# Performance work log

Measured on AMD Instinct MI355X. Metric: run time of the kernel, lower is better.

The kernel has to match this reference:

```python
import jax, jax.numpy as jnp
import numpy as np

B, U, D = 128, 200, 512

def setup_inputs() -> dict:
    key = jax.random.key(0)
    k1, k2, k3 = jax.random.split(key, 3)
    input_real = jax.random.normal(k1, (B, D, D), dtype=jnp.float32)
    input_imag = jax.random.normal(k2, (B, D, D), dtype=jnp.float32)
    # keras 'uniform' initializer: U(-0.05, 0.05); unit_norm constraint normalizes over axes (1,2)
    kernel = jax.random.uniform(k3, (U, D, 2), dtype=jnp.float32, minval=-0.05, maxval=0.05)
    kernel = kernel / jnp.linalg.norm(kernel.reshape(U, -1), axis=1)[:, None, None]
    return {"input_real": input_real, "input_imag": input_imag, "kernel": kernel}

def reference(input_real, input_imag, kernel):
    # kernel: [U, D, 2] -> real/imag measurement vectors
    kr = kernel[:, :, 0]  # [U, D]
    ki = kernel[:, :, 1]  # [U, D]
    # Original: M_real = kr kr^T - ki ki^T ; M_imag = ki kr^T + kr ki^T (outer products per unit)
    # out[b,n] = trace(R_b @ M_real_n) - trace(I_b @ M_imag_n)
    # trace(A @ (u v^T)) = sum_ij A[i,j] u[j] v[i] -> quadratic form, avoids [B,U,D,D] tiles.
    t_real = (jnp.einsum('bij,nj,ni->bn', input_real, kr, kr)
              - jnp.einsum('bij,nj,ni->bn', input_real, ki, ki))
    t_imag = (jnp.einsum('bij,nj,ni->bn', input_imag, ki, kr)
              + jnp.einsum('bij,nj,ni->bn', input_imag, kr, ki))
    return t_real - t_imag  # [B, U]
```

## Files before the change

kernel.cpp:

```cpp
#include <hip/hip_runtime.h>
#include <hip/hip_bf16.h>
#include <string.h>

#define BB 128
#define UU 200
#define DD 512
#define NP 256

typedef __attribute__((ext_vector_type(8))) short short8;
typedef __attribute__((ext_vector_type(4))) float f32x4;
typedef __attribute__((ext_vector_type(16))) float f32x16;

__device__ __forceinline__ unsigned pack_bf16_2(float a, float b) {
    __hip_bfloat162 h = __float22bfloat162_rn(make_float2(a, b));
    unsigned u; memcpy(&u, &h, 4); return u;
}

__device__ __forceinline__ unsigned short f2bf(float x) {
    union { float f; unsigned u; } v; v.f = x;
    unsigned r = v.u + 0x7FFFu + ((v.u >> 16) & 1u);
    return (unsigned short)(r >> 16);
}

__device__ __forceinline__ void glds16(const float* g, float* l) {
    __builtin_amdgcn_global_load_lds(
        (const __attribute__((address_space(1))) unsigned*)g,
        (__attribute__((address_space(3))) unsigned*)l, 16, 0, 0);
}

__global__ void kb2_build_kernel(const float* __restrict__ Kt,
                                 unsigned short* __restrict__ Kbr,
                                 unsigned short* __restrict__ Kbi,
                                 float* __restrict__ out) {
    int idx = blockIdx.x * 256 + threadIdx.x;
    int n = idx >> 9, j = idx & 511;
    unsigned short r = 0, im = 0;
    if (n < UU) {
        float2 s = ((const float2*)Kt)[(size_t)n * DD + j];
        r = f2bf(s.x); im = f2bf(s.y);
    }
    Kbr[idx] = r;
    Kbi[idx] = im;
    if (idx < BB * UU) out[idx] = 0.0f;
}

__global__ void zero_out_kernel(float* __restrict__ out) {
    int i = blockIdx.x * 256 + threadIdx.x;
    if (i < BB * UU) out[i] = 0.0f;
}

__global__ __launch_bounds__(512, 5) void qf_gemm_kernel(
    const float* __restrict__ Ar, const float* __restrict__ Ai,
    const float* __restrict__ Kt,
    const unsigned short* __restrict__ Kbr, const unsigned short* __restrict__ Kbi,
    float* __restrict__ out)
{
    __shared__ float sAf[2][2][32 * 64];

    const int tid  = threadIdx.x;
    const int bx   = blockIdx.x;
    const int b    = bx >> 4;
    const int i0   = (bx & 15) * 32;

    const int w    = tid >> 6;
    const int lane = tid & 63;
    const int l31  = lane & 31;
    const int h    = lane >> 5;
    const int key  = l31 & 15;

    const int srow = w * 4 + (lane >> 4);
    const int scol = (lane & 15) ^ (srow & 15);
    const float* gR = Ar + ((size_t)b * DD + i0 + srow) * DD + scol * 4;
    const float* gI = Ai + ((size_t)b * DD + i0 + srow) * DD + scol * 4;
    const int ldsbase = w * 4 * 64;

    const unsigned short* kbrp = Kbr + (size_t)(w * 32 + l31) * 512 + h * 8;
    const unsigned short* kbip = Kbi + (size_t)(w * 32 + l31) * 512 + h * 8;

    const int rb = l31 * 64;
    int off0[4];
#pragma unroll
    for (int ks = 0; ks < 4; ++ks) {
        int c0 = ks * 4 + 2 * h;
        off0[ks] = rb + ((c0 ^ key) << 2);
    }

    f32x16 accr, acci;
#pragma unroll
    for (int e = 0; e < 16; ++e) { accr[e] = 0.f; acci[e] = 0.f; }

    glds16(gR, &sAf[0][0][ldsbase]);
    glds16(gI, &sAf[0][1][ldsbase]);

#pragma unroll 2
    for (int ss = 0; ss < 8; ++ss) {
        __syncthreads();
        const float* bufR = &sAf[ss & 1][0][0];
        const float* bufI = &sAf[ss & 1][1][0];

        short8 kr[4], ki[4];
        if (w < 7) {
            const unsigned short* krp = kbrp + ss * 64;
            const unsigned short* kip = kbip + ss * 64;
#pragma unroll
            for (int ks = 0; ks < 4; ++ks) {
                kr[ks] = *(const short8*)(krp + ks * 16);
                ki[ks] = *(const short8*)(kip + ks * 16);
            }
        }
        __builtin_amdgcn_sched_barrier(0);

        if (ss < 7) {
            glds16(gR + (ss + 1) * 64, &sAf[(ss + 1) & 1][0][ldsbase]);
            glds16(gI + (ss + 1) * 64, &sAf[(ss + 1) & 1][1][ldsbase]);
        }

        if (w < 7) {
#pragma unroll
            for (int ks = 0; ks < 4; ++ks) {
                const int o0 = off0[ks], o1 = off0[ks] ^ 4;
                f32x4 a0 = *(const f32x4*)&bufR[o0];
                f32x4 a1 = *(const f32x4*)&bufR[o1];
                f32x4 b0 = *(const f32x4*)&bufI[o0];
                f32x4 b1 = *(const f32x4*)&bufI[o1];
                union { short8 v; unsigned u[4]; } fr, fi, nk;
                fr.u[0] = pack_bf16_2(a0[0], a0[1]);
                fr.u[1] = pack_bf16_2(a0[2], a0[3]);
                fr.u[2] = pack_bf16_2(a1[0], a1[1]);
                fr.u[3] = pack_bf16_2(a1[2], a1[3]);
                fi.u[0] = pack_bf16_2(b0[0], b0[1]);
                fi.u[1] = pack_bf16_2(b0[2], b0[3]);
                fi.u[2] = pack_bf16_2(b1[0], b1[1]);
                fi.u[3] = pack_bf16_2(b1[2], b1[3]);
                nk.v = ki[ks];
#pragma unroll
                for (int e = 0; e < 4; ++e) nk.u[e] ^= 0x80008000u;
                accr = __builtin_amdgcn_mfma_f32_32x32x16_bf16(fr.v, kr[ks], accr, 0, 0, 0);
                acci = __builtin_amdgcn_mfma_f32_32x32x16_bf16(fr.v, ki[ks], acci, 0, 0, 0);
                accr = __builtin_amdgcn_mfma_f32_32x32x16_bf16(fi.v, nk.v, accr, 0, 0, 0);
                acci = __builtin_amdgcn_mfma_f32_32x32x16_bf16(fi.v, kr[ks], acci, 0, 0, 0);
            }
        }
    }

    if (w < 7) {
        const int n = w * 32 + l31;
        float s = 0.f;
        if (n < UU) {
            const float* kp = Kt + ((size_t)n * DD + i0 + 4 * h) * 2;
#pragma unroll
            for (int q = 0; q < 4; ++q) {
                f32x4 k01 = *(const f32x4*)(kp + q * 16);
                f32x4 k23 = *(const f32x4*)(kp + q * 16 + 4);
                s += accr[q * 4 + 0] * k01[0] - acci[q * 4 + 0] * k01[1];
                s += accr[q * 4 + 1] * k01[2] - acci[q * 4 + 1] * k01[3];
                s += accr[q * 4 + 2] * k23[0] - acci[q * 4 + 2] * k23[1];
                s += accr[q * 4 + 3] * k23[2] - acci[q * 4 + 3] * k23[3];
            }
        }
        s += __shfl_xor(s, 32, 64);
        if (h == 0 && n < UU)
            atomicAdd(&out[(size_t)b * UU + n], s);
    }
}

#define ASTR 40
#define WSTR 40
__global__ __launch_bounds__(512, 4) void cm_gemm_fb_kernel(
    const float* __restrict__ Ar, const float* __restrict__ Ai,
    const float* __restrict__ Kt, float* __restrict__ dst)
{
    __shared__ short sAr[BB * ASTR];
    __shared__ short sAi[BB * ASTR];
    __shared__ short sWr[NP * WSTR];
    __shared__ short sWi[NP * WSTR];
    const int tid = threadIdx.x, irow = blockIdx.x;
    const int w = tid >> 6, lane = tid & 63;
    const int mw = (w & 1) * 64, nw = (w >> 1) * 64;
    const int rrow = lane & 15, quad = lane >> 4;
    const int nW = tid >> 1, jh = (tid & 1) * 16;
    float krI = 0.f, kiI = 0.f;
    if (nW < UU) { float2 s = ((const float2*)Kt)[(size_t)nW * DD + irow]; krI = s.x; kiI = s.y; }
    const int brow0 = tid >> 3, grp = tid & 7;
    const size_t aoff0 = (size_t)brow0 * DD * DD + (size_t)irow * DD + (size_t)grp * 4;
    const size_t aoff1 = aoff0 + (size_t)64 * DD * DD;
    f32x4 acc[4][4];
#pragma unroll
    for (int a = 0; a < 4; ++a)
#pragma unroll
        for (int c = 0; c < 4; ++c) acc[a][c] = (f32x4)(0.f);
    for (int jw = 0; jw < DD; jw += 32) {
        f32x4 vr0 = *(const f32x4*)(Ar + aoff0 + jw);
        f32x4 vr1 = *(const f32x4*)(Ar + aoff1 + jw);
        f32x4 vi0 = *(const f32x4*)(Ai + aoff0 + jw);
        f32x4 vi1 = *(const f32x4*)(Ai + aoff1 + jw);
        union { unsigned short s[4]; uint2 u; } t0, t1, t2, t3;
#pragma unroll
        for (int q = 0; q < 4; ++q) {
            t0.s[q] = f2bf(vr0[q]); t1.s[q] = f2bf(vr1[q]);
            t2.s[q] = f2bf(vi0[q]); t3.s[q] = f2bf(vi1[q]);
        }
        *(uint2*)&sAr[ brow0       * ASTR + grp * 4] = t0.u;
        *(uint2*)&sAr[(brow0 + 64) * ASTR + grp * 4] = t1.u;
        *(uint2*)&sAi[ brow0       * ASTR + grp * 4] = t2.u;
        *(uint2*)&sAi[(brow0 + 64) * ASTR + grp * 4] = t3.u;
        if (nW < UU) {
            const f32x4* kv = (const f32x4*)(Kt + (size_t)nW * DD * 2 + (size_t)(jw + jh) * 2);
#pragma unroll
            for (int q = 0; q < 8; ++q) {
                f32x4 v = kv[q];
                float wr0 = krI * v[0] - kiI * v[1], wi0 = -(krI * v[1] + kiI * v[0]);
                float wr1 = krI * v[2] - kiI * v[3], wi1 = -(krI * v[3] + kiI * v[2]);
                *(unsigned*)&sWr[nW * WSTR + jh + 2 * q] = (unsigned)f2bf(wr0) | ((unsigned)f2bf(wr1) << 16);
                *(unsigned*)&sWi[nW * WSTR + jh + 2 * q] = (unsigned)f2bf(wi0) | ((unsigned)f2bf(wi1) << 16);
            }
        } else {
#pragma unroll
            for (int q = 0; q < 8; ++q) {
                *(unsigned*)&sWr[nW * WSTR + jh + 2 * q] = 0u;
                *(unsigned*)&sWi[nW * WSTR + jh + 2 * q] = 0u;
            }
        }
        __syncthreads();
#pragma unroll
        for (int ph = 0; ph < 2; ++ph) {
            const short* sA = ph ? sAi : sAr;
            const short* sW = ph ? sWi : sWr;
            short8 af[4], bf[4];
#pragma unroll
            for (int t = 0; t < 4; ++t) {
                af[t] = *(const short8*)&sA[(mw + t * 16 + rrow) * ASTR + quad * 8];
                bf[t] = *(const short8*)&sW[(nw + t * 16 + rrow) * WSTR + quad * 8];
            }
#pragma unroll
            for (int ti = 0; ti < 4; ++ti)
#pragma unroll
                for (int tj = 0; tj < 4; ++tj)
                    acc[ti][tj] = __builtin_amdgcn_mfma_f32_16x16x32_bf16(af[ti], bf[tj], acc[ti][tj], 0, 0, 0);
        }
        __syncthreads();
    }
#pragma unroll
    for (int ti = 0; ti < 4; ++ti) {
        int m = mw + ti * 16 + quad * 4;
#pragma unroll
        for (int tj = 0; tj < 4; ++tj) {
            int n = nw + tj * 16 + rrow;
            if (n < UU)
#pragma unroll
                for (int r = 0; r < 4; ++r)
                    atomicAdd(&dst[(size_t)(m + r) * UU + n], acc[ti][tj][r]);
        }
    }
}

extern "C" void kernel_launch(void* const* d_in, const int* in_sizes, int n_in,
                              void* d_out, int out_size, void* d_ws, size_t ws_size,
                              hipStream_t stream) {
    const float* Ar = (const float*)d_in[0];
    const float* Ai = (const float*)d_in[1];
    const float* Kt = (const float*)d_in[2];
    float* out = (float*)d_out;

    const size_t kb_need = (size_t)2 * NP * DD * sizeof(unsigned short);

    if (ws_size >= kb_need) {
        unsigned short* Kbr = (unsigned short*)d_ws;
        unsigned short* Kbi = Kbr + (size_t)NP * DD;
        hipLaunchKernelGGL(kb2_build_kernel, dim3(512), dim3(256), 0, stream, Kt, Kbr, Kbi, out);
        hipLaunchKernelGGL(qf_gemm_kernel, dim3(2048), dim3(512), 0, stream,
                           Ar, Ai, Kt, Kbr, Kbi, out);
    } else {
        hipLaunchKernelGGL(zero_out_kernel, dim3(100), dim3(256), 0, stream, out);
        hipLaunchKernelGGL(cm_gemm_fb_kernel, dim3(DD), dim3(512), 0, stream, Ar, Ai, Kt, out);
    }
}
```

Baseline: 378.6 us.

## Convert input tile to bf16 once at LDS store and register-prefetch pipeline

Replaces the direct global-to-LDS fp32 loads with register prefetch of the next tile. Each thread converts its four elements to bf16 once and writes them into a swizzled bf16 LDS buffer, so the seven compute waves no longer each re-read fp32 and re-pack it. Kernel fragments are double-buffered in registers in two halves, and the loop is fully unrolled with a custom barrier. This halves LDS footprint and removes redundant conversion work, at the cost of more registers (launch bounds lowered to 4) and exposing global load latency through registers instead of async LDS loads.

```diff
diff --git a/kernel.cpp b/kernel.cpp
--- a/kernel.cpp
+++ b/kernel.cpp
@@ -22,11 +22,13 @@
     return (unsigned short)(r >> 16);
 }
 
-__device__ __forceinline__ void glds16(const float* g, float* l) {
-    __builtin_amdgcn_global_load_lds(
-        (const __attribute__((address_space(1))) unsigned*)g,
-        (__attribute__((address_space(3))) unsigned*)l, 16, 0, 0);
-}
+#define QF_BAR()                                              \
+    do {                                                      \
+        __builtin_amdgcn_sched_barrier(0);                    \
+        asm volatile("s_waitcnt lgkmcnt(0)" ::: "memory");    \
+        __builtin_amdgcn_s_barrier();                         \
+        __builtin_amdgcn_sched_barrier(0);                    \
+    } while (0)
 
 __global__ void kb2_build_kernel(const float* __restrict__ Kt,
                                  unsigned short* __restrict__ Kbr,
@@ -49,13 +51,13 @@
     if (i < BB * UU) out[i] = 0.0f;
 }
 
-__global__ __launch_bounds__(512, 5) void qf_gemm_kernel(
+__global__ __launch_bounds__(512, 4) void qf_gemm_kernel(
     const float* __restrict__ Ar, const float* __restrict__ Ai,
     const float* __restrict__ Kt,
     const unsigned short* __restrict__ Kbr, const unsigned short* __restrict__ Kbi,
     float* __restrict__ out)
 {
-    __shared__ float sAf[2][2][32 * 64];
+    __shared__ __align__(16) short sB[2][2][32 * 64];
 
     const int tid  = threadIdx.x;
     const int bx   = blockIdx.x;
@@ -66,80 +68,115 @@
     const int lane = tid & 63;
     const int l31  = lane & 31;
     const int h    = lane >> 5;
-    const int key  = l31 & 15;
-
-    const int srow = w * 4 + (lane >> 4);
-    const int scol = (lane & 15) ^ (srow & 15);
-    const float* gR = Ar + ((size_t)b * DD + i0 + srow) * DD + scol * 4;
-    const float* gI = Ai + ((size_t)b * DD + i0 + srow) * DD + scol * 4;
-    const int ldsbase = w * 4 * 64;
+
+    const int r0 = tid >> 4;
+    const int g  = tid & 15;
+    const float* gR = Ar + ((size_t)b * DD + i0 + r0) * DD + g * 4;
+    const float* gI = Ai + ((size_t)b * DD + i0 + r0) * DD + g * 4;
+    const int wa = r0 * 64 + ((((g >> 1) ^ (r0 & 7))) << 3) + (g & 1) * 4;
+
+    int roff[4];
+#pragma unroll
+    for (int ks = 0; ks < 4; ++ks)
+        roff[ks] = l31 * 64 + ((((ks << 1) + h) ^ (l31 & 7)) << 3);
 
     const unsigned short* kbrp = Kbr + (size_t)(w * 32 + l31) * 512 + h * 8;
     const unsigned short* kbip = Kbi + (size_t)(w * 32 + l31) * 512 + h * 8;
 
-    const int rb = l31 * 64;
-    int off0[4];
-#pragma unroll
-    for (int ks = 0; ks < 4; ++ks) {
-        int c0 = ks * 4 + 2 * h;
-        off0[ks] = rb + ((c0 ^ key) << 2);
-    }
-
     f32x16 accr, acci;
 #pragma unroll
     for (int e = 0; e < 16; ++e) { accr[e] = 0.f; acci[e] = 0.f; }
 
-    glds16(gR, &sAf[0][0][ldsbase]);
-    glds16(gI, &sAf[0][1][ldsbase]);
-
-#pragma unroll 2
+    short8 kAr[2], kAi[2], kBr[2], kBi[2];
+    f32x4 pfR, pfI;
+
+    if (w < 7) {
+        kAr[0] = *(const short8*)(kbrp +  0);
+        kAi[0] = *(const short8*)(kbip +  0);
+        kAr[1] = *(const short8*)(kbrp + 16);
+        kAi[1] = *(const short8*)(kbip + 16);
+        kBr[0] = *(const short8*)(kbrp + 32);
+        kBi[0] = *(const short8*)(kbip + 32);
+        kBr[1] = *(const short8*)(kbrp + 48);
+        kBi[1] = *(const short8*)(kbip + 48);
+    }
+    pfR = *(const f32x4*)gR;
+    pfI = *(const f32x4*)gI;
+    {
+        uint2 u;
+        u.x = pack_bf16_2(pfR[0], pfR[1]); u.y = pack_bf16_2(pfR[2], pfR[3]);
+        *(uint2*)&sB[0][0][wa] = u;
+        u.x = pack_bf16_2(pfI[0], pfI[1]); u.y = pack_bf16_2(pfI[2], pfI[3]);
+        *(uint2*)&sB[0][1][wa] = u;
+    }
+    pfR = *(const f32x4*)(gR + 64);
+    pfI = *(const f32x4*)(gI + 64);
+    QF_BAR();
+
+#pragma unroll
     for (int ss = 0; ss < 8; ++ss) {
-        __syncthreads();
-        const float* bufR = &sAf[ss & 1][0][0];
-        const float* bufI = &sAf[ss & 1][1][0];
-
-        short8 kr[4], ki[4];
+        const short* bufR = &sB[ss & 1][0][0];
+        const short* bufI = &sB[ss & 1][1][0];
+
         if (w < 7) {
-            const unsigned short* krp = kbrp + ss * 64;
-            const unsigned short* kip = kbip + ss * 64;
-#pragma unroll
-            for (int ks = 0; ks < 4; ++ks) {
-                kr[ks] = *(const short8*)(krp + ks * 16);
-                ki[ks] = *(const short8*)(kip + ks * 16);
-            }
-        }
-        __builtin_amdgcn_sched_barrier(0);
+#pragma unroll
+            for (int ks = 0; ks < 2; ++ks) {
+                short8 ar = *(const short8*)&bufR[roff[ks]];
+                short8 ai = *(const short8*)&bufI[roff[ks]];
+                union { short8 v; unsigned u[4]; } nk;
+                nk.v = kAi[ks];
+#pragma unroll
+                for (int e = 0; e < 4; ++e) nk.u[e] ^= 0x80008000u;
+                accr = __builtin_amdgcn_mfma_f32_32x32x16_bf16(ar, kAr[ks], accr, 0, 0, 0);
+                acci = __builtin_amdgcn_mfma_f32_32x32x16_bf16(ar, kAi[ks], acci, 0, 0, 0);
+                accr = __builtin_amdgcn_mfma_f32_32x32x16_bf16(ai, nk.v,    accr, 0, 0, 0);
+                acci = __builtin_amdgcn_mfma_f32_32x32x16_bf16(ai, kAr[ks], acci, 0, 0, 0);
+            }
+            if (ss < 7) {
+                const unsigned short* krp = kbrp + (ss + 1) * 64;
+                const unsigned short* kip = kbip + (ss + 1) * 64;
+                kAr[0] = *(const short8*)(krp +  0);
+                kAi[0] = *(const short8*)(kip +  0);
+                kAr[1] = *(const short8*)(krp + 16);
+                kAi[1] = *(const short8*)(kip + 16);
+            }
+        }
+
+        if (w < 7) {
+#pragma unroll
+            for (int ks = 0; ks < 2; ++ks) {
+                short8 ar = *(const short8*)&bufR[roff[2 + ks]];
+                short8 ai = *(const short8*)&bufI[roff[2 + ks]];
+                union { short8 v; unsigned u[4]; } nk;
+                nk.v = kBi[ks];
+#pragma unroll
+                for (int e = 0; e < 4; ++e) nk.u[e] ^= 0x80008000u;
+                accr = __builtin_amdgcn_mfma_f32_32x32x16_bf16(ar, kBr[ks], accr, 0, 0, 0);
+                acci = __builtin_amdgcn_mfma_f32_32x32x16_bf16(ar, kBi[ks], acci, 0, 0, 0);
+                accr = __builtin_amdgcn_mfma_f32_32x32x16_bf16(ai, nk.v,    accr, 0, 0, 0);
+                acci = __builtin_amdgcn_mfma_f32_32x32x16_bf16(ai, kBr[ks], acci, 0, 0, 0);
+            }
+            if (ss < 7) {
+                const unsigned short* krp = kbrp + (ss + 1) * 64;
+                const unsigned short* kip = kbip + (ss + 1) * 64;
+                kBr[0] = *(const short8*)(krp + 32);
+                kBi[0] = *(const short8*)(kip + 32);
+                kBr[1] = *(const short8*)(krp + 48);
+                kBi[1] = *(const short8*)(kip + 48);
+            }
+        }
 
         if (ss < 7) {
-            glds16(gR + (ss + 1) * 64, &sAf[(ss + 1) & 1][0][ldsbase]);
-            glds16(gI + (ss + 1) * 64, &sAf[(ss + 1) & 1][1][ldsbase]);
-        }
-
-        if (w < 7) {
-#pragma unroll
-            for (int ks = 0; ks < 4; ++ks) {
-                const int o0 = off0[ks], o1 = off0[ks] ^ 4;
-                f32x4 a0 = *(const f32x4*)&bufR[o0];
-                f32x4 a1 = *(const f32x4*)&bufR[o1];
-                f32x4 b0 = *(const f32x4*)&bufI[o0];
-                f32x4 b1 = *(const f32x4*)&bufI[o1];
-                union { short8 v; unsigned u[4]; } fr, fi, nk;
-                fr.u[0] = pack_bf16_2(a0[0], a0[1]);
-                fr.u[1] = pack_bf16_2(a0[2], a0[3]);
-                fr.u[2] = pack_bf16_2(a1[0], a1[1]);
-                fr.u[3] = pack_bf16_2(a1[2], a1[3]);
-                fi.u[0] = pack_bf16_2(b0[0], b0[1]);
-                fi.u[1] = pack_bf16_2(b0[2], b0[3]);
-                fi.u[2] = pack_bf16_2(b1[0], b1[1]);
-                fi.u[3] = pack_bf16_2(b1[2], b1[3]);
-                nk.v = ki[ks];
-#pragma unroll
-                for (int e = 0; e < 4; ++e) nk.u[e] ^= 0x80008000u;
-                accr = __builtin_amdgcn_mfma_f32_32x32x16_bf16(fr.v, kr[ks], accr, 0, 0, 0);
-                acci = __builtin_amdgcn_mfma_f32_32x32x16_bf16(fr.v, ki[ks], acci, 0, 0, 0);
-                accr = __builtin_amdgcn_mfma_f32_32x32x16_bf16(fi.v, nk.v, accr, 0, 0, 0);
-                acci = __builtin_amdgcn_mfma_f32_32x32x16_bf16(fi.v, kr[ks], acci, 0, 0, 0);
-            }
+            uint2 u;
+            u.x = pack_bf16_2(pfR[0], pfR[1]); u.y = pack_bf16_2(pfR[2], pfR[3]);
+            *(uint2*)&sB[(ss + 1) & 1][0][wa] = u;
+            u.x = pack_bf16_2(pfI[0], pfI[1]); u.y = pack_bf16_2(pfI[2], pfI[3]);
+            *(uint2*)&sB[(ss + 1) & 1][1][wa] = u;
+            if (ss < 6) {
+                pfR = *(const f32x4*)(gR + (ss + 2) * 64);
+                pfI = *(const f32x4*)(gI + (ss + 2) * 64);
+            }
+            QF_BAR();
         }
     }
 
```

New measurement: 349.9 us. 7.6% less time.
